# Kernel optimization log

Hardware: AMD Instinct MI355X
Metric: run time of the kernel (lower is better)

## Reference

```python
import jax, jax.numpy as jnp
import numpy as np

# Config mirrors CrossAttentionAudio2T(dim=768, n_head=12, num_frames=16, spec_frames=8,
# attn_all_frame=True, audio_patch=196, time_encoding=False, use_stpos=True)
B, T, N, NA, ST, D, H = 4, 8, 196, 196, 8, 768, 12
HD = D // H
SCALE = HD ** -0.5


def setup_inputs() -> dict:
    key = jax.random.key(0)
    ks = jax.random.split(key, 12)
    r = lambda k, s: jax.random.normal(k, s, dtype=jnp.float32)
    return dict(
        t_x=r(ks[0], (B, T * N, D)),
        audio=r(ks[1], (NA + 2, B * ST, D)),
        vmae_space_pos=SCALE * r(ks[2], (N, D)),
        audio_space_pos=SCALE * r(ks[3], (NA, D)),
        vmae_temporal_pos=SCALE * r(ks[4], (T, D)),
        audio_temporal_pos=SCALE * r(ks[5], (ST, D)),
        q_w=0.02 * r(ks[6], (D, D)),
        q_b=jnp.zeros((D,), jnp.float32),
        kv_w=0.02 * r(ks[7], (2 * D, D)),
        kv_b=jnp.zeros((2 * D,), jnp.float32),
        proj_w=0.02 * r(ks[8], (D, D)),
        proj_b=jnp.zeros((D,), jnp.float32),
    )


def reference(t_x, audio, vmae_space_pos, audio_space_pos, vmae_temporal_pos,
              audio_temporal_pos, q_w, q_b, kv_w, kv_b, proj_w, proj_b):
    # --- video query tokens: add spatial + temporal pos embeds ---
    x = t_x.reshape(B, T, N, D) + vmae_space_pos          # [B,T,N,D] + [N,D]
    x = x.transpose(0, 2, 1, 3) + vmae_temporal_pos       # [B,N,T,D] + [T,D]
    x = x.transpose(0, 2, 1, 3).reshape(B, T * N, D)      # 'b n t d -> b (t n) d'

    # --- audio key/value tokens: drop 2 lead tokens, add pos embeds ---
    a = audio[2:].reshape(NA, B, ST, D).transpose(1, 2, 0, 3)  # 'n (b t) d -> b t n d'
    a = a + audio_space_pos                                    # [B,ST,NA,D] + [NA,D]
    a = a.transpose(0, 2, 1, 3) + audio_temporal_pos           # [B,NA,ST,D] + [ST,D]
    a = a.reshape(B, NA * ST, D)                               # 'b n t d -> b (n t) d'

    # --- projections ---
    q = (x @ q_w.T + q_b).reshape(B, T * N, H, HD).transpose(0, 2, 1, 3)   # [B,H,Lq,HD]
    kv = (a @ kv_w.T + kv_b).reshape(B, NA * ST, 2, H, HD)
    k = kv[:, :, 0].transpose(0, 2, 1, 3)                                  # [B,H,Lk,HD]
    v = kv[:, :, 1].transpose(0, 2, 1, 3)

    # --- scaled dot-product cross-attention (full score matrix, as in source) ---
    attn = jax.nn.softmax(jnp.einsum('bhqd,bhkd->bhqk', q * SCALE, k), axis=-1)
    o = jnp.einsum('bhqk,bhkd->bhqd', attn, v)
    o = o.transpose(0, 2, 1, 3).reshape(B, T * N, D)
    return o @ proj_w.T + proj_b
```

## Files before the change

kernel.cpp:

```cpp
#include <hip/hip_runtime.h>

typedef short s8v __attribute__((ext_vector_type(8)));
typedef short s4v __attribute__((ext_vector_type(4)));
typedef float f4v __attribute__((ext_vector_type(4)));

#define LQ 1568
#define LK 1568
#define NH 12
#define LQP 1664

__device__ __forceinline__ unsigned short f2bf(float f) {
  union { float f; unsigned u; } x; x.f = f;
  unsigned r = x.u + 0x7FFFu + ((x.u >> 16) & 1u);
  return (unsigned short)(r >> 16);
}
__device__ __forceinline__ float bf2f(unsigned short s) {
  union { unsigned u; float f; } x; x.u = ((unsigned)s) << 16;
  return x.f;
}

__global__ void prep_all(const float* __restrict__ t_x, const float* __restrict__ audio,
                         const float* __restrict__ sp, const float* __restrict__ asp,
                         const float* __restrict__ tp, const float* __restrict__ atp,
                         const float* __restrict__ q_w, const float* __restrict__ kv_w,
                         const float* __restrict__ proj_w,
                         unsigned short* __restrict__ xb, unsigned short* __restrict__ ab,
                         unsigned short* __restrict__ wq, unsigned short* __restrict__ wkv,
                         unsigned short* __restrict__ wp, int total4) {
  const int n1 = 768 * 768 / 4, n2 = 1536 * 768 / 4;
  const int nconv = 2 * n1 + n2;
  int i = blockIdx.x * 256 + threadIdx.x;
  if (i < nconv) {
    const float* src; unsigned short* dst; int j = i;
    if (i < n1)           { src = q_w;    dst = wq;  }
    else if (i < n1 + n2) { src = kv_w;   dst = wkv; j = i - n1; }
    else                  { src = proj_w; dst = wp;  j = i - n1 - n2; }
    float4 v = *(const float4*)(src + (size_t)j * 4);
    ushort4 o;
    o.x = f2bf(v.x); o.y = f2bf(v.y); o.z = f2bf(v.z); o.w = f2bf(v.w);
    *(ushort4*)(dst + (size_t)j * 4) = o;
    return;
  }
  i -= nconv;
  if (i >= 2 * total4) return;
  if (i < total4) {
    int d4 = (i % 192) * 4;
    int row = i / 192;
    int l = row % LQ;
    int t = l / 196, n = l % 196;
    float4 a  = *(const float4*)(t_x + (size_t)i * 4);
    float4 s  = *(const float4*)(sp + n * 768 + d4);
    float4 tt = *(const float4*)(tp + t * 768 + d4);
    ushort4 o;
    o.x = f2bf(a.x + s.x + tt.x);
    o.y = f2bf(a.y + s.y + tt.y);
    o.z = f2bf(a.z + s.z + tt.z);
    o.w = f2bf(a.w + s.w + tt.w);
    *(ushort4*)(xb + (size_t)i * 4) = o;
  } else {
    i -= total4;
    int d4 = (i % 192) * 4;
    int row = i / 192;
    int b = row / LK;
    int r2 = row % LK;
    int na = r2 >> 3, ta = r2 & 7;
    const float* src = audio + ((size_t)(2 + na) * 32 + b * 8 + ta) * 768 + d4;
    float4 a  = *(const float4*)src;
    float4 s  = *(const float4*)(asp + na * 768 + d4);
    float4 tt = *(const float4*)(atp + ta * 768 + d4);
    ushort4 o;
    o.x = f2bf(a.x + s.x + tt.x);
    o.y = f2bf(a.y + s.y + tt.y);
    o.z = f2bf(a.z + s.z + tt.z);
    o.w = f2bf(a.w + s.w + tt.w);
    *(ushort4*)(ab + (size_t)i * 4) = o;
  }
}

__device__ __forceinline__ void gemm_mainloop(
    const unsigned short* __restrict__ A, const unsigned short* __restrict__ W,
    int K, int row0, int col0,
    unsigned short* As, unsigned short* Bs, f4v acc[4][4]) {
  const int tid = threadIdx.x;
  const int lane = tid & 63, wave = tid >> 6;
  const int wm = wave & 1, wn = wave >> 1;
  const int l15 = lane & 15, quad = lane >> 4;
  const int lr = tid >> 3, lc = (tid & 7) * 8;

  for (int k0 = 0; k0 < K; k0 += 64) {
    __syncthreads();
#pragma unroll
    for (int it = 0; it < 4; ++it) {
      int row = lr + it * 32;
      __builtin_amdgcn_global_load_lds(
          (const __attribute__((address_space(1))) unsigned int*)(A + (size_t)(row0 + row) * K + k0 + lc),
          (__attribute__((address_space(3))) unsigned int*)(As + row * 64 + lc), 16, 0, 0);
      __builtin_amdgcn_global_load_lds(
          (const __attribute__((address_space(1))) unsigned int*)(W + (size_t)(col0 + row) * K + k0 + lc),
          (__attribute__((address_space(3))) unsigned int*)(Bs + row * 64 + lc), 16, 0, 0);
    }
    __syncthreads();
#pragma unroll
    for (int kk = 0; kk < 2; ++kk) {
      s8v af[4], bf[4];
#pragma unroll
      for (int i = 0; i < 4; ++i) {
        af[i] = *(const s8v*)(As + (wm * 64 + i * 16 + l15) * 64 + kk * 32 + quad * 8);
        bf[i] = *(const s8v*)(Bs + (wn * 64 + i * 16 + l15) * 64 + kk * 32 + quad * 8);
      }
#pragma unroll
      for (int mi = 0; mi < 4; ++mi)
#pragma unroll
        for (int ni = 0; ni < 4; ++ni)
          acc[mi][ni] = __builtin_amdgcn_mfma_f32_16x16x32_bf16(af[mi], bf[ni],
                                                               acc[mi][ni], 0, 0, 0);
    }
  }
}

__global__ __launch_bounds__(256, 4) void gemm_qkv(
    const unsigned short* __restrict__ xb, const unsigned short* __restrict__ ab,
    const unsigned short* __restrict__ wq, const unsigned short* __restrict__ wkv,
    const float* __restrict__ q_b, const float* __restrict__ kv_b,
    unsigned short* __restrict__ Qs, unsigned short* __restrict__ Kb,
    unsigned short* __restrict__ Vb) {
  __shared__ __align__(16) unsigned short As[128 * 64];
  __shared__ __align__(16) unsigned short Bs[128 * 64];
  const int tid = threadIdx.x;
  const int lane = tid & 63, wave = tid >> 6;
  const int wm = wave & 1, wn = wave >> 1;
  const int l15 = lane & 15, quad = lane >> 4;
  const int row0 = blockIdx.x * 128;
  const int y = blockIdx.y;
  const bool isQ = (y < 6);
  const int col0 = (isQ ? y : y - 6) * 128;
  const unsigned short* A = isQ ? xb : ab;
  const unsigned short* W = isQ ? wq : wkv;
  const float* bias = isQ ? q_b : kv_b;

  f4v acc[4][4] = {};
  gemm_mainloop(A, W, 768, row0, col0, As, Bs, acc);

#pragma unroll
  for (int mi = 0; mi < 4; ++mi) {
    int rowg = row0 + wm * 64 + mi * 16 + quad * 4;
#pragma unroll
    for (int ni = 0; ni < 4; ++ni) {
      int colg = col0 + wn * 64 + ni * 16 + l15;
      float bv = bias[colg];
      if (!isQ && colg >= 768) {
        int oo = colg - 768;
        int h = oo >> 6, hd = oo & 63;
        int b = rowg / LK, l0 = rowg - b * LK;
        ushort4 pk;
        pk.x = f2bf(acc[mi][ni][0] + bv);
        pk.y = f2bf(acc[mi][ni][1] + bv);
        pk.z = f2bf(acc[mi][ni][2] + bv);
        pk.w = f2bf(acc[mi][ni][3] + bv);
        *(ushort4*)(Vb + ((((size_t)b * NH + h) * 392 + (l0 >> 2)) * 64 + hd) * 4) = pk;
        continue;
      }
#pragma unroll
      for (int r = 0; r < 4; ++r) {
        float v = acc[mi][ni][r] + bv;
        int row = rowg + r;
        int b = row / LQ, l = row - b * LQ;
        int h = colg >> 6, hd = colg & 63;
        if (isQ) {
          v *= 0.18033688011112042f;
          Qs[(((size_t)b * NH + h) * LQ + l) * 64 + hd] = f2bf(v);
        } else {
          int tile = l / 112, rr = l - tile * 112;
          Kb[(((size_t)b * NH + h) * 14 + tile) * 8064 + rr * 72 + hd] = f2bf(v);
        }
      }
    }
  }
}

__global__ __launch_bounds__(256, 4) void gemm_proj(
    const unsigned short* __restrict__ A, const unsigned short* __restrict__ W,
    const float* __restrict__ bias, float* __restrict__ out) {
  __shared__ __align__(16) unsigned short As[128 * 64];
  __shared__ __align__(16) unsigned short Bs[128 * 64];
  const int tid = threadIdx.x;
  const int lane = tid & 63, wave = tid >> 6;
  const int wm = wave & 1, wn = wave >> 1;
  const int l15 = lane & 15, quad = lane >> 4;
  const int row0 = blockIdx.x * 128;
  const int col0 = blockIdx.y * 128;

  f4v acc[4][4] = {};
  gemm_mainloop(A, W, 768, row0, col0, As, Bs, acc);

#pragma unroll
  for (int mi = 0; mi < 4; ++mi) {
    int rowg = row0 + wm * 64 + mi * 16 + quad * 4;
#pragma unroll
    for (int ni = 0; ni < 4; ++ni) {
      int colg = col0 + wn * 64 + ni * 16 + l15;
      float bv = bias[colg];
#pragma unroll
      for (int r = 0; r < 4; ++r)
        out[(size_t)(rowg + r) * 768 + colg] = acc[mi][ni][r] + bv;
    }
  }
}

__global__ __launch_bounds__(256, 4) void attn(
    const unsigned short* __restrict__ Q, const unsigned short* __restrict__ Kg,
    const unsigned short* __restrict__ Vsw,
    unsigned short* __restrict__ Op, float* __restrict__ Lp, int Z) {
  __shared__ __align__(16) unsigned short Kl[112 * 72];
  __shared__ __align__(16) unsigned short Vl[112 * 64];
  const int tid = threadIdx.x;
  const int lane = tid & 63, wave = tid >> 6;
  const int l15 = lane & 15, quad = lane >> 4;
  const int bh = blockIdx.y;
  const int q0 = blockIdx.x * 128;
  const int z = blockIdx.z;
  const int t0 = (z * 14) / Z, t1 = ((z + 1) * 14) / Z;
  const size_t base = (size_t)bh * LK * 64;

  s8v qf[2][2];
#pragma unroll
  for (int mt = 0; mt < 2; ++mt)
#pragma unroll
    for (int kk = 0; kk < 2; ++kk) {
      int row = q0 + wave * 32 + mt * 16 + l15;
      if (row > LQ - 1) row = LQ - 1;
      qf[mt][kk] = *(const s8v*)(Q + base + (size_t)row * 64 + kk * 32 + quad * 8);
    }

  f4v of[2][4] = {};
  float lr[2] = {0.0f, 0.0f};

  for (int kt = t0; kt < t1; ++kt) {
    __syncthreads();
    const unsigned short* Ksrc = Kg + ((size_t)bh * 14 + kt) * 8064;
    for (int c = tid; c < 1008; c += 256)
      __builtin_amdgcn_global_load_lds(
          (const __attribute__((address_space(1))) unsigned int*)(Ksrc + c * 8),
          (__attribute__((address_space(3))) unsigned int*)(Kl + c * 8), 16, 0, 0);
    const unsigned short* Vsrc = Vsw + base + (size_t)kt * 112 * 64;
    for (int c = tid; c < 896; c += 256)
      __builtin_amdgcn_global_load_lds(
          (const __attribute__((address_space(1))) unsigned int*)(Vsrc + c * 8),
          (__attribute__((address_space(3))) unsigned int*)(Vl + c * 8), 16, 0, 0);
    __syncthreads();

#pragma unroll
    for (int nt = 0; nt < 7; ++nt) {
      s8v kf0 = *(const s8v*)(Kl + (nt * 16 + l15) * 72 + quad * 8);
      s8v kf1 = *(const s8v*)(Kl + (nt * 16 + l15) * 72 + 32 + quad * 8);
      s4v pf[2];
#pragma unroll
      for (int mt = 0; mt < 2; ++mt) {
        f4v s = {};
        s = __builtin_amdgcn_mfma_f32_16x16x32_bf16(kf0, qf[mt][0], s, 0, 0, 0);
        s = __builtin_amdgcn_mfma_f32_16x16x32_bf16(kf1, qf[mt][1], s, 0, 0, 0);
        float p0 = __builtin_amdgcn_exp2f(s[0]);
        float p1 = __builtin_amdgcn_exp2f(s[1]);
        float p2 = __builtin_amdgcn_exp2f(s[2]);
        float p3 = __builtin_amdgcn_exp2f(s[3]);
        lr[mt] += (p0 + p1) + (p2 + p3);
        union { float f; unsigned u; } a0, a1, a2, a3;
        a0.f = p0; a1.f = p1; a2.f = p2; a3.f = p3;
        union { uint2 u; s4v s; } pk;
        pk.u.x = __builtin_amdgcn_perm(a1.u, a0.u, 0x07060302u);
        pk.u.y = __builtin_amdgcn_perm(a3.u, a2.u, 0x07060302u);
        pf[mt] = pk.s;
      }
#pragma unroll
      for (int nd = 0; nd < 4; ++nd) {
        s4v vf = *(const s4v*)(Vl + ((nt * 4 + quad) << 8) + ((nd * 16 + l15) << 2));
        of[0][nd] = __builtin_amdgcn_mfma_f32_16x16x16bf16_1k(pf[0], vf, of[0][nd], 0, 0, 0);
        of[1][nd] = __builtin_amdgcn_mfma_f32_16x16x16bf16_1k(pf[1], vf, of[1][nd], 0, 0, 0);
      }
    }
  }

#pragma unroll
  for (int mt = 0; mt < 2; ++mt) {
    lr[mt] += __shfl_xor(lr[mt], 16);
    lr[mt] += __shfl_xor(lr[mt], 32);
  }

  const size_t obase = ((size_t)(z * 48 + bh) * LQP + q0);
#pragma unroll
  for (int mt = 0; mt < 2; ++mt) {
#pragma unroll
    for (int r = 0; r < 4; ++r) {
      int rowl = wave * 32 + mt * 16 + quad * 4 + r;
#pragma unroll
      for (int nd = 0; nd < 4; ++nd)
        Op[(obase + rowl) * 64 + nd * 16 + l15] = f2bf(of[mt][nd][r]);
    }
    if (quad == 0)
      Lp[obase + wave * 32 + mt * 16 + l15] = lr[mt];
  }
}

__global__ void attn_merge(const unsigned short* __restrict__ Op,
                           const float* __restrict__ Lp,
                           unsigned short* __restrict__ Om, int Z) {
  int i = blockIdx.x * 256 + threadIdx.x;
  if (i >= 48 * LQ * 8) return;
  int hd8 = (i & 7) * 8;
  int t = i >> 3;
  int row = t % LQ;
  int bh = t / LQ;
  int b = bh / NH, h = bh - b * NH;
  float acc[8] = {};
  float lsum = 0.0f;
  for (int z = 0; z < Z; ++z) {
    size_t rb = (size_t)(z * 48 + bh) * LQP + row;
    lsum += Lp[rb];
    const unsigned short* p = Op + rb * 64 + hd8;
    ushort4 a0 = *(const ushort4*)p, a1 = *(const ushort4*)(p + 4);
    acc[0] += bf2f(a0.x); acc[1] += bf2f(a0.y); acc[2] += bf2f(a0.z); acc[3] += bf2f(a0.w);
    acc[4] += bf2f(a1.x); acc[5] += bf2f(a1.y); acc[6] += bf2f(a1.z); acc[7] += bf2f(a1.w);
  }
  float inv = 1.0f / lsum;
  ushort4 o0, o1;
  o0.x = f2bf(acc[0] * inv); o0.y = f2bf(acc[1] * inv);
  o0.z = f2bf(acc[2] * inv); o0.w = f2bf(acc[3] * inv);
  o1.x = f2bf(acc[4] * inv); o1.y = f2bf(acc[5] * inv);
  o1.z = f2bf(acc[6] * inv); o1.w = f2bf(acc[7] * inv);
  unsigned short* dst = Om + ((size_t)(b * LQ) + row) * 768 + h * 64 + hd8;
  *(ushort4*)dst = o0;
  *(ushort4*)(dst + 4) = o1;
}

extern "C" void kernel_launch(void* const* d_in, const int* in_sizes, int n_in,
                              void* d_out, int out_size, void* d_ws, size_t ws_size,
                              hipStream_t stream) {
  const float* t_x    = (const float*)d_in[0];
  const float* audio  = (const float*)d_in[1];
  const float* sp     = (const float*)d_in[2];
  const float* asp    = (const float*)d_in[3];
  const float* tp     = (const float*)d_in[4];
  const float* atp    = (const float*)d_in[5];
  const float* q_w    = (const float*)d_in[6];
  const float* q_b    = (const float*)d_in[7];
  const float* kv_w   = (const float*)d_in[8];
  const float* kv_b   = (const float*)d_in[9];
  const float* proj_w = (const float*)d_in[10];
  const float* proj_b = (const float*)d_in[11];
  float* out = (float*)d_out;

  char* ws = (char*)d_ws;
  size_t off = 0;
  auto alloc = [&](size_t bytes) -> void* {
    void* p = ws + off;
    off += (bytes + 255) & ~(size_t)255;
    return p;
  };
  const size_t TOK = 6272;
  unsigned short* xb  = (unsigned short*)alloc(TOK * 768 * 2);
  unsigned short* ab  = (unsigned short*)alloc(TOK * 768 * 2);
  unsigned short* wq  = (unsigned short*)alloc(768 * 768 * 2);
  unsigned short* wkv = (unsigned short*)alloc(1536 * 768 * 2);
  unsigned short* wp  = (unsigned short*)alloc(768 * 768 * 2);
  unsigned short* Qs  = (unsigned short*)alloc(TOK * 768 * 2);
  unsigned short* Kb  = (unsigned short*)alloc((size_t)48 * 14 * 8064 * 2);
  unsigned short* Vb  = (unsigned short*)alloc(TOK * 768 * 2);

  auto need = [&](int Z) {
    return off + (size_t)Z * 48 * LQP * 64 * 2 + (size_t)Z * 48 * LQP * 4 + 512;
  };
  int Z;
  unsigned short* Op;
  float* Lp;
  if (ws_size >= need(7)) {
    Z = 7;
    Op = (unsigned short*)alloc((size_t)7 * 48 * LQP * 64 * 2);
    Lp = (float*)alloc((size_t)7 * 48 * LQP * 4);
  } else if (ws_size >= need(4)) {
    Z = 4;
    Op = (unsigned short*)alloc((size_t)4 * 48 * LQP * 64 * 2);
    Lp = (float*)alloc((size_t)4 * 48 * LQP * 4);
  } else {
    Z = 2;
    Op = (unsigned short*)ws;
    Lp = (float*)(ws + (size_t)2 * 48 * LQP * 64 * 2);
  }
  unsigned short* Om = Qs;

  dim3 blk(256);
  const int n1 = 768 * 768 / 4, n2 = 1536 * 768 / 4;
  int total4 = (int)(TOK * 192);
  int nprep = 2 * n1 + n2 + 2 * total4;
  prep_all<<<dim3((nprep + 255) / 256), blk, 0, stream>>>(
      t_x, audio, sp, asp, tp, atp, q_w, kv_w, proj_w, xb, ab, wq, wkv, wp, total4);

  gemm_qkv<<<dim3(49, 18), blk, 0, stream>>>(xb, ab, wq, wkv, q_b, kv_b, Qs, Kb, Vb);

  attn<<<dim3(13, 48, Z), blk, 0, stream>>>(Qs, Kb, Vb, Op, Lp, Z);

  attn_merge<<<dim3((48 * LQ * 8 + 255) / 256), blk, 0, stream>>>(Op, Lp, Om, Z);

  gemm_proj<<<dim3(49, 6), blk, 0, stream>>>(Om, wp, proj_b, out);
}
```

Before: 236.3 us.

## Store attention partials in fragment-native layout, reduce split count, raise occupancy

The attention kernel now writes its partial outputs in MFMA fragment order as packed 8-byte stores instead of scattered 2-byte row-major stores. The merge kernel reads that layout back and does the row-major transpose while normalising. The key split count drops from 7 to 4, which cuts partial-output traffic and merge work. Launch bounds go up to 5 blocks per CU, which may cost registers in the attention kernel.

New measurement: 331.8 us. 1.4x slower.

```diff
diff --git a/kernel.cpp b/kernel.cpp
--- a/kernel.cpp
+++ b/kernel.cpp
@@ -14,8 +14,8 @@
   unsigned r = x.u + 0x7FFFu + ((x.u >> 16) & 1u);
   return (unsigned short)(r >> 16);
 }
-__device__ __forceinline__ float bf2f(unsigned short s) {
-  union { unsigned u; float f; } x; x.u = ((unsigned)s) << 16;
+__device__ __forceinline__ float bf2f(unsigned s) {
+  union { unsigned u; float f; } x; x.u = s << 16;
   return x.f;
 }
 
@@ -207,7 +207,7 @@
   }
 }
 
-__global__ __launch_bounds__(256, 4) void attn(
+__global__ __launch_bounds__(256, 5) void attn(
     const unsigned short* __restrict__ Q, const unsigned short* __restrict__ Kg,
     const unsigned short* __restrict__ Vsw,
     unsigned short* __restrict__ Op, float* __restrict__ Lp, int Z) {
@@ -286,18 +286,20 @@
     lr[mt] += __shfl_xor(lr[mt], 32);
   }
 
-  const size_t obase = ((size_t)(z * 48 + bh) * LQP + q0);
+  const size_t bbase = (((size_t)z * 48 + bh) * 13 + blockIdx.x) * 8192;
 #pragma unroll
   for (int mt = 0; mt < 2; ++mt) {
 #pragma unroll
-    for (int r = 0; r < 4; ++r) {
-      int rowl = wave * 32 + mt * 16 + quad * 4 + r;
-#pragma unroll
-      for (int nd = 0; nd < 4; ++nd)
-        Op[(obase + rowl) * 64 + nd * 16 + l15] = f2bf(of[mt][nd][r]);
+    for (int nd = 0; nd < 4; ++nd) {
+      union { uint2 u; ushort4 s; } pk;
+      pk.s.x = f2bf(of[mt][nd][0]);
+      pk.s.y = f2bf(of[mt][nd][1]);
+      pk.s.z = f2bf(of[mt][nd][2]);
+      pk.s.w = f2bf(of[mt][nd][3]);
+      *(uint2*)(Op + bbase + (size_t)(((wave * 2 + mt) * 4 + nd) * 256 + lane * 4)) = pk.u;
     }
     if (quad == 0)
-      Lp[obase + wave * 32 + mt * 16 + l15] = lr[mt];
+      Lp[((size_t)z * 48 + bh) * LQP + q0 + wave * 32 + mt * 16 + l15] = lr[mt];
   }
 }
 
@@ -305,31 +307,31 @@
                            const float* __restrict__ Lp,
                            unsigned short* __restrict__ Om, int Z) {
   int i = blockIdx.x * 256 + threadIdx.x;
-  if (i >= 48 * LQ * 8) return;
-  int hd8 = (i & 7) * 8;
-  int t = i >> 3;
-  int row = t % LQ;
-  int bh = t / LQ;
+  int c = i & 2047;
+  int t = i >> 11;
+  int x = t % 13, bh = t / 13;
+  int lane = c & 63, fo = c >> 6;
+  int nd = fo & 3, wm = fo >> 2;
+  int quad = lane >> 4, l15 = lane & 15;
+  int rowl = (wm >> 1) * 32 + (wm & 1) * 16 + quad * 4;
+  int col = nd * 16 + l15;
+  float acc[4] = {};
+  float ls[4] = {};
+  for (int z = 0; z < Z; ++z) {
+    size_t zb = (size_t)z * 48 + bh;
+    uint2 v = *(const uint2*)(Op + (zb * 13 + x) * 8192 + (size_t)c * 4);
+    acc[0] += bf2f(v.x & 0xffffu); acc[1] += bf2f(v.x >> 16);
+    acc[2] += bf2f(v.y & 0xffffu); acc[3] += bf2f(v.y >> 16);
+    float4 lv = *(const float4*)(Lp + zb * LQP + x * 128 + rowl);
+    ls[0] += lv.x; ls[1] += lv.y; ls[2] += lv.z; ls[3] += lv.w;
+  }
   int b = bh / NH, h = bh - b * NH;
-  float acc[8] = {};
-  float lsum = 0.0f;
-  for (int z = 0; z < Z; ++z) {
-    size_t rb = (size_t)(z * 48 + bh) * LQP + row;
-    lsum += Lp[rb];
-    const unsigned short* p = Op + rb * 64 + hd8;
-    ushort4 a0 = *(const ushort4*)p, a1 = *(const ushort4*)(p + 4);
-    acc[0] += bf2f(a0.x); acc[1] += bf2f(a0.y); acc[2] += bf2f(a0.z); acc[3] += bf2f(a0.w);
-    acc[4] += bf2f(a1.x); acc[5] += bf2f(a1.y); acc[6] += bf2f(a1.z); acc[7] += bf2f(a1.w);
-  }
-  float inv = 1.0f / lsum;
-  ushort4 o0, o1;
-  o0.x = f2bf(acc[0] * inv); o0.y = f2bf(acc[1] * inv);
-  o0.z = f2bf(acc[2] * inv); o0.w = f2bf(acc[3] * inv);
-  o1.x = f2bf(acc[4] * inv); o1.y = f2bf(acc[5] * inv);
-  o1.z = f2bf(acc[6] * inv); o1.w = f2bf(acc[7] * inv);
-  unsigned short* dst = Om + ((size_t)(b * LQ) + row) * 768 + h * 64 + hd8;
-  *(ushort4*)dst = o0;
-  *(ushort4*)(dst + 4) = o1;
+#pragma unroll
+  for (int r = 0; r < 4; ++r) {
+    int l = x * 128 + rowl + r;
+    if (l >= LQ) continue;
+    Om[((size_t)b * LQ + l) * 768 + h * 64 + col] = f2bf(acc[r] / ls[r]);
+  }
 }
 
 extern "C" void kernel_launch(void* const* d_in, const int* in_sizes, int n_in,
@@ -366,24 +368,20 @@
   unsigned short* Kb  = (unsigned short*)alloc((size_t)48 * 14 * 8064 * 2);
   unsigned short* Vb  = (unsigned short*)alloc(TOK * 768 * 2);
 
-  auto need = [&](int Z) {
-    return off + (size_t)Z * 48 * LQP * 64 * 2 + (size_t)Z * 48 * LQP * 4 + 512;
+  auto need = [&](int Zq) {
+    return off + (size_t)Zq * 48 * 13 * 8192 * 2 + (size_t)Zq * 48 * LQP * 4 + 512;
   };
   int Z;
   unsigned short* Op;
   float* Lp;
-  if (ws_size >= need(7)) {
-    Z = 7;
-    Op = (unsigned short*)alloc((size_t)7 * 48 * LQP * 64 * 2);
-    Lp = (float*)alloc((size_t)7 * 48 * LQP * 4);
-  } else if (ws_size >= need(4)) {
+  if (ws_size >= need(4)) {
     Z = 4;
-    Op = (unsigned short*)alloc((size_t)4 * 48 * LQP * 64 * 2);
+    Op = (unsigned short*)alloc((size_t)4 * 48 * 13 * 8192 * 2);
     Lp = (float*)alloc((size_t)4 * 48 * LQP * 4);
   } else {
     Z = 2;
     Op = (unsigned short*)ws;
-    Lp = (float*)(ws + (size_t)2 * 48 * LQP * 64 * 2);
+    Lp = (float*)(ws + (size_t)2 * 48 * 13 * 8192 * 2);
   }
   unsigned short* Om = Qs;
 
@@ -398,7 +396,7 @@
 
   attn<<<dim3(13, 48, Z), blk, 0, stream>>>(Qs, Kb, Vb, Op, Lp, Z);
 
-  attn_merge<<<dim3((48 * LQ * 8 + 255) / 256), blk, 0, stream>>>(Op, Lp, Om, Z);
+  attn_merge<<<dim3(48 * 13 * 2048 / 256), blk, 0, stream>>>(Op, Lp, Om, Z);
 
   gemm_proj<<<dim3(49, 6), blk, 0, stream>>>(Om, wp, proj_b, out);
 }
```
